# Kernel optimization log

Measured on AMD Instinct MI355X. Metric: run time of the kernel, lower is better.

Reference implementation:

```python
import jax, jax.numpy as jnp
import numpy as np

NUM_CLASSES = 10
BASE_TEMPERATURE = 0.07
TEMP = 0.1


def setup_inputs() -> dict:
    key = jax.random.key(0)
    k1, k2 = jax.random.split(key)
    features = jax.random.normal(k1, (8192, 128), dtype=jnp.float32)
    targets = jax.random.randint(k2, (8192,), 0, NUM_CLASSES, dtype=jnp.int64)
    return {"features": features, "targets": targets}


def reference(features, targets):
    bs = features.shape[0]
    dtype = features.dtype
    # one-hot label matrix -> positive mask via label agreement
    one_hot = jax.nn.one_hot(targets, NUM_CLASSES, dtype=dtype)          # [bs, C]
    mask_pos_full = one_hot @ one_hot.T                                  # [bs, bs], 1 if same class
    mask_negatives = jnp.ones((bs, bs), dtype=dtype) - mask_pos_full
    mask_positives = mask_pos_full - jnp.eye(bs, dtype=dtype)            # exclude self
    logits_mask = mask_positives + mask_negatives                        # == 1 - eye
    # pairwise similarity logits
    logits = (features @ features.T) / TEMP                              # [bs, bs]
    logits_max = jax.lax.stop_gradient(jnp.max(logits, axis=1, keepdims=True))
    logits = logits - logits_max
    exp_logits = jnp.exp(logits) * logits_mask
    log_prob = logits - jnp.log(jnp.sum(exp_logits, axis=1, keepdims=True) + 1e-20)
    mean_log_prob_pos = jnp.sum(mask_positives * log_prob, axis=1) / (
        jnp.sum(mask_positives, axis=1) + 1e-20
    )
    loss = -(TEMP / BASE_TEMPERATURE) * jnp.mean(mean_log_prob_pos)
    avg_pos = jnp.mean(jnp.sum(mask_positives, axis=1))
    avg_neg = jnp.mean(jnp.sum(mask_negatives, axis=1))
    return (loss, avg_pos, avg_neg)
```

## Files before the change

kernel.cpp:

```cpp
#include <hip/hip_runtime.h>

#define N 8192
#define KD 128
#define NCLS 10
#define GRID 512
#define TPB 256

typedef __attribute__((ext_vector_type(4))) int intx4;


__device__ __forceinline__ float slabmin(const int* __restrict__ Dpart, int slab) {
    float a = fminf(__int_as_float(Dpart[slab * 4 + 0]), __int_as_float(Dpart[slab * 4 + 1]));
    float b = fminf(__int_as_float(Dpart[slab * 4 + 2]), __int_as_float(Dpart[slab * 4 + 3]));
    return fminf(a, b);
}

__device__ __forceinline__ void st_agent(int* p, int v) {
    __hip_atomic_store(p, v, __ATOMIC_RELAXED, __HIP_MEMORY_SCOPE_AGENT);
}
__device__ __forceinline__ void st_agent_f(float* p, float v) {
    __hip_atomic_store(p, v, __ATOMIC_RELAXED, __HIP_MEMORY_SCOPE_AGENT);
}
__device__ __forceinline__ float ld_agent_f(const float* p) {
    return __hip_atomic_load(p, __ATOMIC_RELAXED, __HIP_MEMORY_SCOPE_AGENT);
}
__device__ __forceinline__ int ld_agent(const int* p) {
    return __hip_atomic_load(p, __ATOMIC_RELAXED, __HIP_MEMORY_SCOPE_AGENT);
}
__device__ __forceinline__ int fadd_agent(int* p) {
    return __hip_atomic_fetch_add(p, 1, __ATOMIC_RELAXED, __HIP_MEMORY_SCOPE_AGENT);
}

__device__ __forceinline__ void release_flags(int* flagv, int epoch) {
#pragma unroll
    for (int i = 0; i < 8; ++i) st_agent(&flagv[i * 32], epoch);
}
__device__ __forceinline__ void wait_flag(const int* flagv, int b, int epoch) {
    while (ld_agent(&flagv[(b & 7) * 32]) < epoch) __builtin_amdgcn_s_sleep(2);
}
__device__ __forceinline__ void arrive_tree(int* grp, int* root, int* flagv, int b, int thr_grp,
                                            int thr_root, int epoch) {
    if (fadd_agent(&grp[(b >> 3) * 32]) == thr_grp)
        if (fadd_agent(root) == thr_root) release_flags(flagv, epoch);
}

__global__ __launch_bounds__(TPB, 2) void k_fused(const float* __restrict__ F,
                                                  const int* __restrict__ tgt,
                                                  float* __restrict__ diag10,
                                                  int* __restrict__ Q,
                                                  float* __restrict__ S,
                                                  int* __restrict__ cnt,
                                                  float* __restrict__ PS,
                                                  int* __restrict__ Dpart,
                                                  float* __restrict__ accg,
                                                  int* __restrict__ grp,
                                                  int* __restrict__ root,
                                                  int* __restrict__ flagv,
                                                  float* __restrict__ out) {
    const unsigned char* Qb = (const unsigned char*)Q;
    int b = blockIdx.x;
    int t = threadIdx.x;

    __shared__ int bmin;
    __shared__ union {
        struct { int lh[NCLS]; float red[2][NCLS][KD]; } cls;
        struct { float Ss[NCLS * KD]; int cs[NCLS]; float wsum[4]; } fin;
    } sh;

    {
        int row0 = b * 16;
        if (t == 0) bmin = 0x7f7fffff;
        __syncthreads();
        if (t < 16) st_agent_f(&PS[row0 + t], 0.f);
        int col4 = t & 31;
        int rg = t >> 5;
#pragma unroll
        for (int sw = 0; sw < 2; ++sw) {
            int row = row0 + sw * 8 + rg;
            float4 v = *(const float4*)(F + (size_t)row * KD + col4 * 4);
            float sq = v.x * v.x + v.y * v.y + v.z * v.z + v.w * v.w;
#pragma unroll
            for (int off = 16; off >= 1; off >>= 1) sq += __shfl_xor(sq, off);
            if (col4 == 0) {
                float dg = 10.f * sq;
                st_agent_f(&diag10[row], dg);
                atomicMin(&bmin, __float_as_int(dg));
            }
            int q0 = __float2int_rn(30.f * fminf(fmaxf(v.x, -4.2f), 4.2f));
            int q1 = __float2int_rn(30.f * fminf(fmaxf(v.y, -4.2f), 4.2f));
            int q2 = __float2int_rn(30.f * fminf(fmaxf(v.z, -4.2f), 4.2f));
            int q3 = __float2int_rn(30.f * fminf(fmaxf(v.w, -4.2f), 4.2f));
            int dq = (q0 & 255) | ((q1 & 255) << 8) | ((q2 & 255) << 16) | ((q3 & 255) << 24);
            int idx = (row >> 4) * 512 + (col4 >> 4) * 256 + ((col4 >> 2) & 3) * 64 +
                      (row & 15) * 4 + (col4 & 3);
            st_agent(&Q[idx], dq);
        }
        __syncthreads();
        if (t == 0) {
            st_agent(&Dpart[b], bmin);
            asm volatile("s_waitcnt vmcnt(0)" ::: "memory");
            arrive_tree(grp, root, flagv, b, 7, 63, 1);
        }
    }

    if (b < 128) {
        int row0 = b * 64;
        int k = t & 127, h = t >> 7;
        if (t < NCLS) sh.cls.lh[t] = 0;
        __syncthreads();
        if (t < 64) atomicAdd(&sh.cls.lh[tgt[row0 + t]], 1);
        float local[NCLS];
#pragma unroll
        for (int c = 0; c < NCLS; ++c) local[c] = 0.f;
        for (int ii = 0; ii < 32; ++ii) {
            int row = row0 + h * 32 + ii;
            float v = F[(size_t)row * KD + k];
            int c = tgt[row];
#pragma unroll
            for (int cc = 0; cc < NCLS; ++cc) local[cc] += (cc == c) ? v : 0.f;
        }
#pragma unroll
        for (int cc = 0; cc < NCLS; ++cc) sh.cls.red[h][cc][k] = local[cc];
        __syncthreads();
        if (h == 0) {
#pragma unroll
            for (int cc = 0; cc < NCLS; ++cc)
                atomicAdd(&S[cc * KD + k], sh.cls.red[0][cc][k] + sh.cls.red[1][cc][k]);
            if (t < NCLS) atomicAdd(&cnt[t], sh.cls.lh[t]);
        }
    }

    if (t == 0) wait_flag(flagv, b, 1);
    __syncthreads();

    {
        int bx = b & 127, y = b >> 7;
        int w = t >> 6, lane = t & 63;
        int quad = lane >> 4, l16 = lane & 15;
        int row0 = bx * 64;

        float dmr = slabmin(Dpart, bx);

        intx4 af[4][2];
#pragma unroll
        for (int it = 0; it < 4; ++it)
#pragma unroll
            for (int ks = 0; ks < 2; ++ks)
                af[it][ks] =
                    *(const intx4*)(Qb + (size_t)(bx * 4 + it) * 2048 + ks * 1024 + lane * 16);

        bool ext = (y == 0) && (bx < 64) && (w == 0);

        intx4 bufs[2][4][2];
        {
            int col0 = ((bx + y * 16 + w) & 127) * 64;
            const unsigned char* bp = Qb + (size_t)(col0 >> 4) * 2048 + lane * 16;
#pragma unroll
            for (int tj = 0; tj < 4; ++tj)
#pragma unroll
                for (int ks = 0; ks < 2; ++ks)
                    bufs[0][tj][ks] = *(const intx4*)(bp + tj * 2048 + ks * 1024);
        }

#pragma unroll
        for (int s = 0; s < 4; ++s) {
            if (s < 3) {
                int coln = ((bx + y * 16 + (s + 1) * 4 + w) & 127) * 64;
                const unsigned char* bp = Qb + (size_t)(coln >> 4) * 2048 + lane * 16;
#pragma unroll
                for (int tj = 0; tj < 4; ++tj)
#pragma unroll
                    for (int ks = 0; ks < 2; ++ks)
                        bufs[(s + 1) & 1][tj][ks] = *(const intx4*)(bp + tj * 2048 + ks * 1024);
            } else if (ext) {
                int coln = (bx + 64) * 64;
                const unsigned char* bp = Qb + (size_t)(coln >> 4) * 2048 + lane * 16;
#pragma unroll
                for (int tj = 0; tj < 4; ++tj)
#pragma unroll
                    for (int ks = 0; ks < 2; ++ks)
                        bufs[0][tj][ks] = *(const intx4*)(bp + tj * 2048 + ks * 1024);
            }

            int csb = (bx + y * 16 + s * 4 + w) & 127;
            int col0 = csb * 64;
            int thrq = (int)((fminf(dmr, slabmin(Dpart, csb)) - 60.f) * 90.f);

            intx4 acc[4][4];
#pragma unroll
            for (int it = 0; it < 4; ++it)
#pragma unroll
                for (int tj = 0; tj < 4; ++tj)
                    acc[it][tj] = (intx4){0, 0, 0, 0};
#pragma unroll
            for (int ks = 0; ks < 2; ++ks)
#pragma unroll
                for (int it = 0; it < 4; ++it)
#pragma unroll
                    for (int tj = 0; tj < 4; ++tj)
                        acc[it][tj] = __builtin_amdgcn_mfma_i32_16x16x64_i8(
                            af[it][ks], bufs[s & 1][tj][ks], acc[it][tj], 0, 0, 0);

            int mx = -2147483647;
#pragma unroll
            for (int it = 0; it < 4; ++it)
#pragma unroll
                for (int tj = 0; tj < 4; ++tj) {
                    int a01 = max(acc[it][tj][0], acc[it][tj][1]);
                    int a23 = max(acc[it][tj][2], acc[it][tj][3]);
                    mx = max(mx, max(a01, a23));
                }

            if (__any(mx > thrq)) {
                bool has_diag = (col0 == row0);
#pragma unroll
                for (int it = 0; it < 4; ++it)
#pragma unroll
                    for (int r = 0; r < 4; ++r) {
                        int grow = row0 + it * 16 + quad * 4 + r;
                        float Mrow = diag10[grow];
                        float rs = 0.f;
#pragma unroll
                        for (int tj = 0; tj < 4; ++tj) {
                            int gcol = col0 + tj * 16 + l16;
                            float lv = (float)acc[it][tj][r] * (1.f / 90.f);
                            float ev = __expf(lv - Mrow);
                            rs += (grow == gcol) ? 0.f : ev;
                        }
                        rs += __shfl_xor(rs, 1, 16);
                        rs += __shfl_xor(rs, 2, 16);
                        rs += __shfl_xor(rs, 4, 16);
                        rs += __shfl_xor(rs, 8, 16);
                        if (l16 == 0) atomicAdd(&PS[grow], rs);
                    }
                if (!has_diag) {
#pragma unroll
                    for (int tj = 0; tj < 4; ++tj) {
                        int gcol = col0 + tj * 16 + l16;
                        float Mcol = diag10[gcol];
                        float cs_ = 0.f;
#pragma unroll
                        for (int it = 0; it < 4; ++it)
#pragma unroll
                            for (int r = 0; r < 4; ++r)
                                cs_ += __expf((float)acc[it][tj][r] * (1.f / 90.f) - Mcol);
                        cs_ += __shfl_xor(cs_, 16);
                        cs_ += __shfl_xor(cs_, 32);
                        if (quad == 0) atomicAdd(&PS[gcol], cs_);
                    }
                }
            }
        }

        if (ext) {
            int col0 = (bx + 64) * 64;
            int thrq = (int)((fminf(dmr, slabmin(Dpart, bx + 64)) - 60.f) * 90.f);
            intx4 acc[4][4];
#pragma unroll
            for (int it = 0; it < 4; ++it)
#pragma unroll
                for (int tj = 0; tj < 4; ++tj)
                    acc[it][tj] = (intx4){0, 0, 0, 0};
#pragma unroll
            for (int ks = 0; ks < 2; ++ks)
#pragma unroll
                for (int it = 0; it < 4; ++it)
#pragma unroll
                    for (int tj = 0; tj < 4; ++tj)
                        acc[it][tj] = __builtin_amdgcn_mfma_i32_16x16x64_i8(
                            af[it][ks], bufs[0][tj][ks], acc[it][tj], 0, 0, 0);

            int mx = -2147483647;
#pragma unroll
            for (int it = 0; it < 4; ++it)
#pragma unroll
                for (int tj = 0; tj < 4; ++tj) {
                    int a01 = max(acc[it][tj][0], acc[it][tj][1]);
                    int a23 = max(acc[it][tj][2], acc[it][tj][3]);
                    mx = max(mx, max(a01, a23));
                }
            if (__any(mx > thrq)) {
#pragma unroll
                for (int it = 0; it < 4; ++it)
#pragma unroll
                    for (int r = 0; r < 4; ++r) {
                        int grow = row0 + it * 16 + quad * 4 + r;
                        float Mrow = diag10[grow];
                        float rs = 0.f;
#pragma unroll
                        for (int tj = 0; tj < 4; ++tj) {
                            float lv = (float)acc[it][tj][r] * (1.f / 90.f);
                            rs += __expf(lv - Mrow);
                        }
                        rs += __shfl_xor(rs, 1, 16);
                        rs += __shfl_xor(rs, 2, 16);
                        rs += __shfl_xor(rs, 4, 16);
                        rs += __shfl_xor(rs, 8, 16);
                        if (l16 == 0) atomicAdd(&PS[grow], rs);
                    }
#pragma unroll
                for (int tj = 0; tj < 4; ++tj) {
                    int gcol = col0 + tj * 16 + l16;
                    float Mcol = diag10[gcol];
                    float cs_ = 0.f;
#pragma unroll
                    for (int it = 0; it < 4; ++it)
#pragma unroll
                        for (int r = 0; r < 4; ++r)
                            cs_ += __expf((float)acc[it][tj][r] * (1.f / 90.f) - Mcol);
                    cs_ += __shfl_xor(cs_, 16);
                    cs_ += __shfl_xor(cs_, 32);
                    if (quad == 0) atomicAdd(&PS[gcol], cs_);
                }
            }
        }
    }

    __syncthreads();
    if (t == 0) {
        asm volatile("s_waitcnt vmcnt(0)" ::: "memory");
        arrive_tree(grp, root, flagv, b, 15, 127, 2);
    }
    if (b >= 128) return;

    {
        int g = t >> 2, q = t & 3;
        int row = b * 64 + g;
        int c = tgt[row];
        float4 ff[8];
#pragma unroll
        for (int i = 0; i < 8; ++i)
            ff[i] = *(const float4*)(F + (size_t)row * KD + i * 16 + q * 4);
        float M = diag10[row];

        if (t == 0) wait_flag(flagv, b, 2);
        __syncthreads();

        for (int i = t; i < NCLS * KD; i += TPB) sh.fin.Ss[i] = ld_agent_f(&S[i]);
        if (t < NCLS) sh.fin.cs[t] = ld_agent(&cnt[t]);
        __syncthreads();

        float dot = 0.f;
#pragma unroll
        for (int i = 0; i < 8; ++i) {
            float4 s = *(const float4*)(sh.fin.Ss + c * KD + i * 16 + q * 4);
            dot += ff[i].x * s.x + ff[i].y * s.y + ff[i].z * s.z + ff[i].w * s.w;
        }
        dot += __shfl_xor(dot, 1, 4);
        dot += __shfl_xor(dot, 2, 4);

        float mlp = 0.f;
        if (q == 0) {
            float pp = 10.f * dot - M;
            float T = ld_agent_f(&PS[row]);
            float np = (float)(sh.fin.cs[c] - 1);
            mlp = (np < 0.5f) ? 0.f : (pp - np * (M + __logf(T + 1e-20f))) / np;
        }
#pragma unroll
        for (int off = 32; off >= 1; off >>= 1) mlp += __shfl_xor(mlp, off);
        int lane = t & 63, w = t >> 6;
        if (lane == 0) sh.fin.wsum[w] = mlp;
        __syncthreads();
        if (t == 0) {
            atomicAdd(accg, (sh.fin.wsum[0] + sh.fin.wsum[1]) + (sh.fin.wsum[2] + sh.fin.wsum[3]));
            asm volatile("s_waitcnt vmcnt(0)" ::: "memory");
            int old = atomicAdd(&cnt[12], 1);
            if (old == 127) {
                float tot = atomicAdd(accg, 0.0f);
                double sp = 0.0, sn = 0.0;
                for (int cc = 0; cc < NCLS; ++cc) {
                    double n = (double)sh.fin.cs[cc];
                    sp += n * (n - 1.0);
                    sn += n * ((double)N - n);
                }
                out[0] = (float)(-(0.1 / 0.07) * ((double)tot / (double)N));
                out[1] = (float)(sp / (double)N);
                out[2] = (float)(sn / (double)N);
            }
        }
    }
}

extern "C" void kernel_launch(void* const* d_in, const int* in_sizes, int n_in,
                              void* d_out, int out_size, void* d_ws, size_t ws_size,
                              hipStream_t stream) {
    const float* F = (const float*)d_in[0];
    const int* tgt = (const int*)d_in[1];
    float* out = (float*)d_out;
    char* ws = (char*)d_ws;

    int* cnt = (int*)(ws);
    float* acc = (float*)(ws + 64);
    float* S = (float*)(ws + 128);
    int* flagv = (int*)(ws + 6144);
    int* root = (int*)(ws + 7168);
    float* PS = (float*)(ws + 8192);
    int* grp = (int*)(ws + 40960);
    int* Dpart = (int*)(ws + 49152);
    float* diag10 = (float*)(ws + 65536);
    int* Q = (int*)(ws + (1u << 20));

    hipMemsetAsync(ws, 0, 49152, stream);
    k_fused<<<GRID, TPB, 0, stream>>>(F, tgt, diag10, Q, S, cnt, PS, Dpart, acc, grp, root,
                                      flagv, out);
}
```

Before: 82.12 us.

## Replace global barrier with per-slab readiness flags and rebalance tile work

The first grid-wide barrier after quantization is replaced by per-64-row slab counters and flags. Each block now waits only for the specific slabs it will read, so blocks can start the int8 MFMA similarity tiles without waiting for the whole grid. Class-sum work moves to the y==2 blocks, which also get fewer tiles (3 versus 4 or 5), to balance load. The ext tile moves to y==1, and the tree barrier is reused once for the final phase. The risk is spinning on many flags and uneven per-block timing. A larger workspace memset is also needed.

```diff
diff --git a/kernel.cpp b/kernel.cpp
--- a/kernel.cpp
+++ b/kernel.cpp
@@ -56,10 +56,13 @@
                                                   int* __restrict__ grp,
                                                   int* __restrict__ root,
                                                   int* __restrict__ flagv,
+                                                  int* __restrict__ slabc,
+                                                  int* __restrict__ slabf,
                                                   float* __restrict__ out) {
     const unsigned char* Qb = (const unsigned char*)Q;
     int b = blockIdx.x;
     int t = threadIdx.x;
+    int bx = b & 127, y = b >> 7;
 
     __shared__ int bmin;
     __shared__ union {
@@ -99,12 +102,12 @@
         if (t == 0) {
             st_agent(&Dpart[b], bmin);
             asm volatile("s_waitcnt vmcnt(0)" ::: "memory");
-            arrive_tree(grp, root, flagv, b, 7, 63, 1);
-        }
-    }
-
-    if (b < 128) {
-        int row0 = b * 64;
+            if (fadd_agent(&slabc[(b >> 2) * 32]) == 3) st_agent(&slabf[(b >> 2) * 32], 1);
+        }
+    }
+
+    if (y == 2) {
+        int row0 = bx * 64;
         int k = t & 127, h = t >> 7;
         if (t < NCLS) sh.cls.lh[t] = 0;
         __syncthreads();
@@ -130,14 +133,35 @@
         }
     }
 
-    if (t == 0) wait_flag(flagv, b, 1);
-    __syncthreads();
-
     {
-        int bx = b & 127, y = b >> 7;
+        int dd = -1;
+        if (y == 0) {
+            if (t < 16) dd = t;
+            else if (t < 20) dd = t + 28;
+        } else if (y == 1) {
+            if (t < 16) dd = 16 + t;
+            else if (t == 16) dd = 0;
+            else if (t == 17 && bx < 64) dd = 64;
+        } else if (y == 2) {
+            if (t < 12) dd = 32 + t;
+            else if (t == 12) dd = 0;
+        } else {
+            if (t < 16) dd = 48 + t;
+            else if (t == 16) dd = 0;
+        }
+        if (dd >= 0) {
+            int s = (bx + dd) & 127;
+            while (!ld_agent(&slabf[s * 32])) __builtin_amdgcn_s_sleep(2);
+        }
+        __syncthreads();
+    }
+
+    {
         int w = t >> 6, lane = t & 63;
         int quad = lane >> 4, l16 = lane & 15;
         int row0 = bx * 64;
+        int nst = (y == 0) ? 5 : ((y == 2) ? 3 : 4);
+        bool ext = (y == 1) && (bx < 64) && (w == 0);
 
         float dmr = slabmin(Dpart, bx);
 
@@ -148,8 +172,6 @@
             for (int ks = 0; ks < 2; ++ks)
                 af[it][ks] =
                     *(const intx4*)(Qb + (size_t)(bx * 4 + it) * 2048 + ks * 1024 + lane * 16);
-
-        bool ext = (y == 0) && (bx < 64) && (w == 0);
 
         intx4 bufs[2][4][2];
         {
@@ -163,90 +185,94 @@
         }
 
 #pragma unroll
-        for (int s = 0; s < 4; ++s) {
-            if (s < 3) {
-                int coln = ((bx + y * 16 + (s + 1) * 4 + w) & 127) * 64;
-                const unsigned char* bp = Qb + (size_t)(coln >> 4) * 2048 + lane * 16;
-#pragma unroll
-                for (int tj = 0; tj < 4; ++tj)
-#pragma unroll
-                    for (int ks = 0; ks < 2; ++ks)
-                        bufs[(s + 1) & 1][tj][ks] = *(const intx4*)(bp + tj * 2048 + ks * 1024);
-            } else if (ext) {
-                int coln = (bx + 64) * 64;
-                const unsigned char* bp = Qb + (size_t)(coln >> 4) * 2048 + lane * 16;
-#pragma unroll
-                for (int tj = 0; tj < 4; ++tj)
-#pragma unroll
-                    for (int ks = 0; ks < 2; ++ks)
-                        bufs[0][tj][ks] = *(const intx4*)(bp + tj * 2048 + ks * 1024);
-            }
-
-            int csb = (bx + y * 16 + s * 4 + w) & 127;
-            int col0 = csb * 64;
-            int thrq = (int)((fminf(dmr, slabmin(Dpart, csb)) - 60.f) * 90.f);
-
-            intx4 acc[4][4];
-#pragma unroll
-            for (int it = 0; it < 4; ++it)
-#pragma unroll
-                for (int tj = 0; tj < 4; ++tj)
-                    acc[it][tj] = (intx4){0, 0, 0, 0};
-#pragma unroll
-            for (int ks = 0; ks < 2; ++ks)
+        for (int s = 0; s < 5; ++s) {
+            if (s < nst) {
+                if (s + 1 < nst) {
+                    int ddn = (s + 1 < 4) ? (y * 16 + (s + 1) * 4 + w) : (44 + w);
+                    int coln = ((bx + ddn) & 127) * 64;
+                    const unsigned char* bp = Qb + (size_t)(coln >> 4) * 2048 + lane * 16;
+#pragma unroll
+                    for (int tj = 0; tj < 4; ++tj)
+#pragma unroll
+                        for (int ks = 0; ks < 2; ++ks)
+                            bufs[(s + 1) & 1][tj][ks] = *(const intx4*)(bp + tj * 2048 + ks * 1024);
+                } else if (ext) {
+                    int coln = (bx + 64) * 64;
+                    const unsigned char* bp = Qb + (size_t)(coln >> 4) * 2048 + lane * 16;
+#pragma unroll
+                    for (int tj = 0; tj < 4; ++tj)
+#pragma unroll
+                        for (int ks = 0; ks < 2; ++ks)
+                            bufs[0][tj][ks] = *(const intx4*)(bp + tj * 2048 + ks * 1024);
+                }
+
+                int dd = (s < 4) ? (y * 16 + s * 4 + w) : (44 + w);
+                int csb = (bx + dd) & 127;
+                int col0 = csb * 64;
+                int thrq = (int)((fminf(dmr, slabmin(Dpart, csb)) - 60.f) * 90.f);
+
+                intx4 acc[4][4];
 #pragma unroll
                 for (int it = 0; it < 4; ++it)
 #pragma unroll
                     for (int tj = 0; tj < 4; ++tj)
-                        acc[it][tj] = __builtin_amdgcn_mfma_i32_16x16x64_i8(
-                            af[it][ks], bufs[s & 1][tj][ks], acc[it][tj], 0, 0, 0);
-
-            int mx = -2147483647;
-#pragma unroll
-            for (int it = 0; it < 4; ++it)
-#pragma unroll
-                for (int tj = 0; tj < 4; ++tj) {
-                    int a01 = max(acc[it][tj][0], acc[it][tj][1]);
-                    int a23 = max(acc[it][tj][2], acc[it][tj][3]);
-                    mx = max(mx, max(a01, a23));
-                }
-
-            if (__any(mx > thrq)) {
-                bool has_diag = (col0 == row0);
+                        acc[it][tj] = (intx4){0, 0, 0, 0};
+#pragma unroll
+                for (int ks = 0; ks < 2; ++ks)
+#pragma unroll
+                    for (int it = 0; it < 4; ++it)
+#pragma unroll
+                        for (int tj = 0; tj < 4; ++tj)
+                            acc[it][tj] = __builtin_amdgcn_mfma_i32_16x16x64_i8(
+                                af[it][ks], bufs[s & 1][tj][ks], acc[it][tj], 0, 0, 0);
+
+                int mx = -2147483647;
 #pragma unroll
                 for (int it = 0; it < 4; ++it)
 #pragma unroll
-                    for (int r = 0; r < 4; ++r) {
-                        int grow = row0 + it * 16 + quad * 4 + r;
-                        float Mrow = diag10[grow];
-                        float rs = 0.f;
+                    for (int tj = 0; tj < 4; ++tj) {
+                        int a01 = max(acc[it][tj][0], acc[it][tj][1]);
+                        int a23 = max(acc[it][tj][2], acc[it][tj][3]);
+                        mx = max(mx, max(a01, a23));
+                    }
+
+                if (__any(mx > thrq)) {
+                    bool has_diag = (col0 == row0);
+#pragma unroll
+                    for (int it = 0; it < 4; ++it)
+#pragma unroll
+                        for (int r = 0; r < 4; ++r) {
+                            int grow = row0 + it * 16 + quad * 4 + r;
+                            float Mrow = diag10[grow];
+                            float rs = 0.f;
+#pragma unroll
+                            for (int tj = 0; tj < 4; ++tj) {
+                                int gcol = col0 + tj * 16 + l16;
+                                float lv = (float)acc[it][tj][r] * (1.f / 90.f);
+                                float ev = __expf(lv - Mrow);
+                                rs += (grow == gcol) ? 0.f : ev;
+                            }
+                            rs += __shfl_xor(rs, 1, 16);
+                            rs += __shfl_xor(rs, 2, 16);
+                            rs += __shfl_xor(rs, 4, 16);
+                            rs += __shfl_xor(rs, 8, 16);
+                            if (l16 == 0) atomicAdd(&PS[grow], rs);
+                        }
+                    if (!has_diag) {
 #pragma unroll
                         for (int tj = 0; tj < 4; ++tj) {
                             int gcol = col0 + tj * 16 + l16;
-                            float lv = (float)acc[it][tj][r] * (1.f / 90.f);
-                            float ev = __expf(lv - Mrow);
-                            rs += (grow == gcol) ? 0.f : ev;
+                            float Mcol = diag10[gcol];
+                            float cs_ = 0.f;
+#pragma unroll
+                            for (int it = 0; it < 4; ++it)
+#pragma unroll
+                                for (int r = 0; r < 4; ++r)
+                                    cs_ += __expf((float)acc[it][tj][r] * (1.f / 90.f) - Mcol);
+                            cs_ += __shfl_xor(cs_, 16);
+                            cs_ += __shfl_xor(cs_, 32);
+                            if (quad == 0) atomicAdd(&PS[gcol], cs_);
                         }
-                        rs += __shfl_xor(rs, 1, 16);
-                        rs += __shfl_xor(rs, 2, 16);
-                        rs += __shfl_xor(rs, 4, 16);
-                        rs += __shfl_xor(rs, 8, 16);
-                        if (l16 == 0) atomicAdd(&PS[grow], rs);
-                    }
-                if (!has_diag) {
-#pragma unroll
-                    for (int tj = 0; tj < 4; ++tj) {
-                        int gcol = col0 + tj * 16 + l16;
-                        float Mcol = diag10[gcol];
-                        float cs_ = 0.f;
-#pragma unroll
-                        for (int it = 0; it < 4; ++it)
-#pragma unroll
-                            for (int r = 0; r < 4; ++r)
-                                cs_ += __expf((float)acc[it][tj][r] * (1.f / 90.f) - Mcol);
-                        cs_ += __shfl_xor(cs_, 16);
-                        cs_ += __shfl_xor(cs_, 32);
-                        if (quad == 0) atomicAdd(&PS[gcol], cs_);
                     }
                 }
             }
@@ -319,7 +345,7 @@
     __syncthreads();
     if (t == 0) {
         asm volatile("s_waitcnt vmcnt(0)" ::: "memory");
-        arrive_tree(grp, root, flagv, b, 15, 127, 2);
+        arrive_tree(grp, root, flagv, b, 7, 63, 1);
     }
     if (b >= 128) return;
 
@@ -333,7 +359,7 @@
             ff[i] = *(const float4*)(F + (size_t)row * KD + i * 16 + q * 4);
         float M = diag10[row];
 
-        if (t == 0) wait_flag(flagv, b, 2);
+        if (t == 0) wait_flag(flagv, b, 1);
         __syncthreads();
 
         for (int i = t; i < NCLS * KD; i += TPB) sh.fin.Ss[i] = ld_agent_f(&S[i]);
@@ -398,9 +424,11 @@
     int* grp = (int*)(ws + 40960);
     int* Dpart = (int*)(ws + 49152);
     float* diag10 = (float*)(ws + 65536);
+    int* slabc = (int*)(ws + 131072);
+    int* slabf = (int*)(ws + 147456);
     int* Q = (int*)(ws + (1u << 20));
 
-    hipMemsetAsync(ws, 0, 49152, stream);
+    hipMemsetAsync(ws, 0, 163840, stream);
     k_fused<<<GRID, TPB, 0, stream>>>(F, tgt, diag10, Q, S, cnt, PS, Dpart, acc, grp, root,
-                                      flagv, out);
-}
+                                      flagv, slabc, slabf, out);
+}
```

Result: no change. 80.59 us (-1.9%).
